# Optimization experiments

Hardware: AMD Instinct MI355X
Metric: run time of the kernel (lower is better)

Reference implementation:

```python
import jax, jax.numpy as jnp
import numpy as np

R = 1024          # number of 'a' tokens merged per sample
PROTECT_CLS = True


def setup_inputs() -> dict:
    key = jax.random.key(0)
    k1, k2 = jax.random.split(key)
    B, T, C = 8, 4096, 512
    x = jax.random.normal(k1, (B, T, C), dtype=jnp.float32)
    k = jax.random.normal(k2, (B, T, C), dtype=jnp.float32)
    return {"x": x, "k": k}


def reference(x, k):
    B, T, C = x.shape
    r = R
    pos_a = jnp.arange(0, T, 2)          # (Ta,)
    pos_b = jnp.arange(1, T, 2)          # (Tb,)
    Tb = pos_b.shape[0]

    # cosine-similarity scores between even ('a') and odd ('b') keys
    a = k[:, ::2, :]
    b = k[:, 1::2, :]
    a = a / (jnp.linalg.norm(a, axis=-1, keepdims=True) + 1e-12)
    b = b / (jnp.linalg.norm(b, axis=-1, keepdims=True) + 1e-12)
    scores = jnp.einsum('bac,bdc->bad', a, b)   # (B, Ta, Tb)
    if PROTECT_CLS:
        scores = scores.at[:, 0, :].set(-jnp.inf)

    node_max = jnp.max(scores, axis=-1)          # (B, Ta)
    node_idx = jnp.argmax(scores, axis=-1)       # (B, Ta) best 'b' partner per 'a'
    edge_order = jnp.argsort(-node_max, axis=-1) # descending
    src_idx = edge_order[:, :r]                  # merged 'a' tokens
    unm_sorted = jnp.sort(edge_order[:, r:], axis=-1)  # unmerged 'a', sorted
    dst_idx = jnp.take_along_axis(node_idx, src_idx, axis=-1)  # (B, r)

    src_tok = x[:, ::2, :]
    dst_tok = x[:, 1::2, :]
    unm = jnp.take_along_axis(src_tok, unm_sorted[..., None], axis=1)      # (B, Ta-r, C)
    src_sel = jnp.take_along_axis(src_tok, src_idx[..., None], axis=1)     # (B, r, C)
    dst_updated = jax.vmap(lambda d, i, s: d.at[i].add(s))(dst_tok, dst_idx, src_sel)
    merged = jnp.concatenate([unm, dst_updated], axis=1)                   # (B, Ta-r+Tb, C)

    base_b = unm.shape[1]
    unm_pos = pos_a[unm_sorted]   # (B, Ta-r) original positions of unmerged 'a'
    src_pos = pos_a[src_idx]      # (B, r)    original positions of merged 'a'

    def build_si(up, sp, di):
        si = jnp.full((T,), -1, dtype=jnp.int32)
        si = si.at[up].set(jnp.arange(base_b, dtype=jnp.int32))
        si = si.at[pos_b].set(base_b + jnp.arange(Tb, dtype=jnp.int32))
        si = si.at[sp].set((base_b + di).astype(jnp.int32))
        return si

    source_index = jax.vmap(build_si)(unm_pos, src_pos, dst_idx)  # (B, T)
    return merged, source_index
```

## Files before the change

kernel.cpp:

```cpp
#include <hip/hip_runtime.h>
#include <stdint.h>

#define BN 8
#define TN 4096
#define CN 512
#define TA 2048
#define RR 1024
#define BASEB 1024
#define MROWS 3072
#define KC 32

typedef _Float16 f16x8 __attribute__((ext_vector_type(8)));
typedef float f32x4 __attribute__((ext_vector_type(4)));
typedef __attribute__((address_space(3))) uint32_t lds_u32_t;
typedef __attribute__((address_space(1))) const uint32_t g_u32_t;

__device__ __forceinline__ unsigned ofloat(float f) {
    unsigned u = __float_as_uint(f);
    return (u & 0x80000000u) ? ~u : (u | 0x80000000u);
}

__global__ __launch_bounds__(256) void split_kernel(const float* __restrict__ k,
        _Float16* __restrict__ Ahi, _Float16* __restrict__ Alo,
        _Float16* __restrict__ Bhi, _Float16* __restrict__ Blo) {
    int row = blockIdx.x * 4 + (threadIdx.x >> 6);
    int lane = threadIdx.x & 63;
    const float* p = k + (size_t)row * CN;
    float4 v1 = *(const float4*)(p + lane * 8);
    float4 v2 = *(const float4*)(p + lane * 8 + 4);
    float s = v1.x*v1.x + v1.y*v1.y + v1.z*v1.z + v1.w*v1.w
            + v2.x*v2.x + v2.y*v2.y + v2.z*v2.z + v2.w*v2.w;
    #pragma unroll
    for (int off = 32; off > 0; off >>= 1) s += __shfl_xor(s, off);
    float sc = 1024.0f / (sqrtf(s) + 1e-12f);
    float m[8] = {v1.x*sc, v1.y*sc, v1.z*sc, v1.w*sc,
                  v2.x*sc, v2.y*sc, v2.z*sc, v2.w*sc};
    f16x8 H, L;
    #pragma unroll
    for (int jj = 0; jj < 8; ++jj) {
        _Float16 h = (_Float16)m[jj];
        H[jj] = h;
        L[jj] = (_Float16)(m[jj] - (float)h);
    }
    int b = row >> 12;
    int tt = row & 4095;
    size_t dst = ((size_t)(b * TA + (tt >> 1))) * CN + lane * 8;
    if (tt & 1) { *(f16x8*)(Bhi + dst) = H; *(f16x8*)(Blo + dst) = L; }
    else        { *(f16x8*)(Ahi + dst) = H; *(f16x8*)(Alo + dst) = L; }
}

__global__ void init_kernel(unsigned long long* __restrict__ nodekey) {
    int idx = blockIdx.x * 256 + threadIdx.x;
    if (idx < BN * TA)
        nodekey[idx] = (((unsigned long long)0x007FFFFFu) << 32) | 0xFFFFFFFFull;
}

__global__ __launch_bounds__(256, 4) void score_mfma_kernel(
        const _Float16* __restrict__ Ahi, const _Float16* __restrict__ Alo,
        const _Float16* __restrict__ Bhi, const _Float16* __restrict__ Blo,
        unsigned long long* __restrict__ nodekey) {
    __shared__ _Float16 lds[4 * 128 * KC];
    const int b  = blockIdx.z;
    const int i0 = blockIdx.x * 128;
    const int j0 = blockIdx.y * 128;
    const int tid = threadIdx.x;
    const int lane = tid & 63;
    const int w = tid >> 6;
    const int wr = (w >> 1) * 64;
    const int wc = (w & 1) * 64;
    const size_t boff = (size_t)b * TA * CN;

    const _Float16* gbase[4] = {
        Ahi + boff + (size_t)i0 * CN,
        Alo + boff + (size_t)i0 * CN,
        Bhi + boff + (size_t)j0 * CN,
        Blo + boff + (size_t)j0 * CN };

    const int srow = tid >> 2;
    const int segD = (tid & 3) ^ ((tid >> 3) & 3);

    f32x4 acc[4][4];
    #pragma unroll
    for (int m = 0; m < 4; ++m)
        #pragma unroll
        for (int n = 0; n < 4; ++n) acc[m][n] = (f32x4){0.f, 0.f, 0.f, 0.f};

    const int fr = lane & 15, ks = lane >> 4;
    int aoff[4], boff2[4];
    #pragma unroll
    for (int m = 0; m < 4; ++m) {
        int r = wr + m * 16 + fr;
        aoff[m] = r * KC + (ks ^ ((r >> 1) & 3)) * 8;
    }
    #pragma unroll
    for (int n = 0; n < 4; ++n) {
        int r = wc + n * 16 + fr;
        boff2[n] = r * KC + (ks ^ ((r >> 1) & 3)) * 8;
    }

    for (int kt = 0; kt < CN; kt += KC) {
        #pragma unroll
        for (int i = 0; i < 8; ++i) {
            const _Float16* gp = gbase[i >> 1]
                + (size_t)((i & 1) * 64 + srow) * CN + kt + segD * 8;
            _Float16* lp = lds + i * 2048 + w * 512;
            __builtin_amdgcn_global_load_lds((g_u32_t*)gp, (lds_u32_t*)lp, 16, 0, 0);
        }
        __syncthreads();
        f16x8 bh[4], bl[4];
        #pragma unroll
        for (int n = 0; n < 4; ++n) {
            bh[n] = *(const f16x8*)(&lds[2 * 4096 + boff2[n]]);
            bl[n] = *(const f16x8*)(&lds[3 * 4096 + boff2[n]]);
        }
        #pragma unroll
        for (int m = 0; m < 4; ++m) {
            f16x8 ah = *(const f16x8*)(&lds[0 * 4096 + aoff[m]]);
            f16x8 al = *(const f16x8*)(&lds[1 * 4096 + aoff[m]]);
            #pragma unroll
            for (int n = 0; n < 4; ++n) {
                acc[m][n] = __builtin_amdgcn_mfma_f32_16x16x32_f16(ah, bh[n], acc[m][n], 0, 0, 0);
                acc[m][n] = __builtin_amdgcn_mfma_f32_16x16x32_f16(ah, bl[n], acc[m][n], 0, 0, 0);
                acc[m][n] = __builtin_amdgcn_mfma_f32_16x16x32_f16(al, bh[n], acc[m][n], 0, 0, 0);
            }
        }
        __syncthreads();
    }

    const float SC = 1.0f / 1048576.0f;
    #pragma unroll
    for (int m = 0; m < 4; ++m) {
        #pragma unroll
        for (int reg = 0; reg < 4; ++reg) {
            unsigned bhi = 0u, blo2 = 0u;
            #pragma unroll
            for (int n = 0; n < 4; ++n) {
                float sc = acc[m][n][reg] * SC;
                unsigned j = (unsigned)(j0 + wc + n * 16 + fr);
                unsigned khi = ofloat(sc), klo = 0xFFFFFFFFu - j;
                if (khi > bhi || (khi == bhi && klo > blo2)) { bhi = khi; blo2 = klo; }
            }
            #pragma unroll
            for (int mm2 = 8; mm2 > 0; mm2 >>= 1) {
                unsigned ohi = (unsigned)__shfl_xor((int)bhi, mm2, 16);
                unsigned olo = (unsigned)__shfl_xor((int)blo2, mm2, 16);
                if (ohi > bhi || (ohi == bhi && olo > blo2)) { bhi = ohi; blo2 = olo; }
            }
            if (fr == 0) {
                int i = i0 + wr + m * 16 + ks * 4 + reg;
                if (i != 0) {
                    unsigned long long key = (((unsigned long long)bhi) << 32) | blo2;
                    atomicMax(&nodekey[b * TA + i], key);
                }
            }
        }
    }
}

__global__ __launch_bounds__(256) void rank_flag_kernel(
        const unsigned long long* __restrict__ nodekey,
        int* __restrict__ is_src) {
    __shared__ unsigned long long K[2048];
    const int b = blockIdx.y;
    const int t = threadIdx.x;
    for (int i = t; i < 2048; i += 256) {
        unsigned hi = (unsigned)(nodekey[b * TA + i] >> 32);
        K[i] = (((unsigned long long)hi) << 32) | (unsigned)(2047 - i);
    }
    __syncthreads();
    const int i = blockIdx.x * 256 + t;
    const unsigned long long ki = K[i];
    int rank = 0;
    #pragma unroll 8
    for (int j = 0; j < 2048; ++j) rank += (K[j] > ki) ? 1 : 0;
    is_src[b * TA + i] = (rank < RR) ? 1 : 0;
}

__global__ __launch_bounds__(1024) void scan_si_kernel(const int* __restrict__ is_src,
        const unsigned long long* __restrict__ nodekey,
        int* __restrict__ unm_rank, float* __restrict__ out_si) {
    __shared__ int ps[2048];
    __shared__ unsigned char fl[2048];
    const int b = blockIdx.x;
    const int t = threadIdx.x;
    int s0 = is_src[b * TA + t];
    int s1 = is_src[b * TA + 1024 + t];
    int f0 = 1 - s0, f1 = 1 - s1;
    fl[t] = (unsigned char)s0;
    fl[t + 1024] = (unsigned char)s1;
    ps[t] = f0;
    ps[t + 1024] = f1;
    __syncthreads();
    for (int off = 1; off < 2048; off <<= 1) {
        int v0 = (t >= off) ? ps[t - off] : 0;
        int v1 = ((t + 1024) >= off) ? ps[t + 1024 - off] : 0;
        __syncthreads();
        ps[t] += v0;
        ps[t + 1024] += v1;
        __syncthreads();
    }
    int u0 = ps[t] - f0, u1 = ps[t + 1024] - f1;
    unm_rank[b * TA + t] = u0;
    unm_rank[b * TA + 1024 + t] = u1;
    #pragma unroll
    for (int h = 0; h < 2; ++h) {
        int i = t + h * 1024;
        int u = h ? u1 : u0;
        int val;
        if (fl[i]) {
            unsigned j = 0xFFFFFFFFu - (unsigned)(nodekey[b * TA + i] & 0xFFFFFFFFull);
            val = BASEB + (int)j;
        } else {
            val = u;
        }
        out_si[(size_t)b * TN + 2 * i]     = (float)val;
        out_si[(size_t)b * TN + 2 * i + 1] = (float)(BASEB + i);
    }
}

__global__ __launch_bounds__(128) void copy_kernel(const float* __restrict__ x,
                                                   const int* __restrict__ is_src,
                                                   const int* __restrict__ unm_rank,
                                                   float* __restrict__ out) {
    const int b = blockIdx.y;
    const int tt = blockIdx.x;
    const float* src;
    float* dst;
    if (tt < 2048) {
        int i = tt;
        if (is_src[b * TA + i]) return;
        src = x + ((size_t)b * TN + 2 * i) * CN;
        dst = out + ((size_t)b * MROWS + unm_rank[b * TA + i]) * CN;
    } else {
        int j = tt - 2048;
        src = x + ((size_t)b * TN + 2 * j + 1) * CN;
        dst = out + ((size_t)b * MROWS + BASEB + j) * CN;
    }
    ((float4*)dst)[threadIdx.x] = ((const float4*)src)[threadIdx.x];
}

__global__ __launch_bounds__(256) void scatter_kernel(const float* __restrict__ x,
                                                      const int* __restrict__ is_src,
                                                      const unsigned long long* __restrict__ nodekey,
                                                      float* __restrict__ out) {
    const int b = blockIdx.y;
    const int i = blockIdx.x;
    if (!is_src[b * TA + i]) return;
    unsigned j = 0xFFFFFFFFu - (unsigned)(nodekey[b * TA + i] & 0xFFFFFFFFull);
    const float* src = x + ((size_t)b * TN + 2 * i) * CN;
    float* dst = out + ((size_t)b * MROWS + BASEB + j) * CN;
    for (int c = threadIdx.x; c < CN; c += 256) atomicAdd(&dst[c], src[c]);
}

extern "C" void kernel_launch(void* const* d_in, const int* in_sizes, int n_in,
                              void* d_out, int out_size, void* d_ws, size_t ws_size,
                              hipStream_t stream) {
    const float* x = (const float*)d_in[0];
    const float* k = (const float*)d_in[1];
    float* out = (float*)d_out;
    float* out_si = out + (size_t)BN * MROWS * CN;

    char* ws = (char*)d_ws;
    const size_t PLANE = (size_t)BN * TA * CN;
    _Float16* Ahi = (_Float16*)ws;
    _Float16* Alo = Ahi + PLANE;
    _Float16* Bhi = Alo + PLANE;
    _Float16* Blo = Bhi + PLANE;
    char* tail = ws + 4 * PLANE * sizeof(_Float16);
    unsigned long long* nodekey = (unsigned long long*)(tail);
    int* is_src   = (int*)(tail + 128 * 1024);
    int* unm_rank = (int*)(tail + 192 * 1024);

    split_kernel<<<dim3(BN * TN / 4), dim3(256), 0, stream>>>(k, Ahi, Alo, Bhi, Blo);
    init_kernel<<<dim3((BN * TA + 255) / 256), dim3(256), 0, stream>>>(nodekey);
    score_mfma_kernel<<<dim3(16, 16, BN), dim3(256), 0, stream>>>(Ahi, Alo, Bhi, Blo, nodekey);
    rank_flag_kernel<<<dim3(8, BN), dim3(256), 0, stream>>>(nodekey, is_src);
    scan_si_kernel<<<dim3(BN), dim3(1024), 0, stream>>>(is_src, nodekey, unm_rank, out_si);
    copy_kernel<<<dim3(4096, BN), dim3(128), 0, stream>>>(x, is_src, unm_rank, out);
    scatter_kernel<<<dim3(2048, BN), dim3(256), 0, stream>>>(x, is_src, nodekey, out);
}
```

Before: 204.8 us.

## Replace split-fp16 3-MFMA scoring with hi-only GEMM plus error-bounded candidate rescore

The score GEMM now uses only the high fp16 part of each normalized key (one MFMA instead of three per tile) and writes a tight row max. Using per-row error bounds built from the hi/lo norms, it keeps up to 64 candidate columns per row that could still be the true argmax. A new rescore kernel recomputes those candidates exactly in fp32 from the original keys, and falls back to a full scan when a row overflows. This cuts MFMA work and the lo-plane memory traffic, but adds candidate atomics, a second pass, and a risk of slow fallback rows.

```diff
diff --git a/kernel.cpp b/kernel.cpp
--- a/kernel.cpp
+++ b/kernel.cpp
@@ -9,6 +9,7 @@
 #define BASEB 1024
 #define MROWS 3072
 #define KC 32
+#define CAP 64
 
 typedef _Float16 f16x8 __attribute__((ext_vector_type(8)));
 typedef float f32x4 __attribute__((ext_vector_type(4)));
@@ -19,10 +20,16 @@
     unsigned u = __float_as_uint(f);
     return (u & 0x80000000u) ? ~u : (u | 0x80000000u);
 }
+__device__ __forceinline__ float unofloat(unsigned u) {
+    unsigned v = (u & 0x80000000u) ? (u ^ 0x80000000u) : ~u;
+    return __uint_as_float(v);
+}
 
 __global__ __launch_bounds__(256) void split_kernel(const float* __restrict__ k,
-        _Float16* __restrict__ Ahi, _Float16* __restrict__ Alo,
-        _Float16* __restrict__ Bhi, _Float16* __restrict__ Blo) {
+        _Float16* __restrict__ Ahi, _Float16* __restrict__ Bhi,
+        float* __restrict__ invA, float* __restrict__ invB,
+        float* __restrict__ nHa, float* __restrict__ nLa,
+        float* __restrict__ Pq, float* __restrict__ Qq) {
     int row = blockIdx.x * 4 + (threadIdx.x >> 6);
     int lane = threadIdx.x & 63;
     const float* p = k + (size_t)row * CN;
@@ -32,34 +39,66 @@
             + v2.x*v2.x + v2.y*v2.y + v2.z*v2.z + v2.w*v2.w;
     #pragma unroll
     for (int off = 32; off > 0; off >>= 1) s += __shfl_xor(s, off);
-    float sc = 1024.0f / (sqrtf(s) + 1e-12f);
+    float inv = 1.0f / (sqrtf(s) + 1e-12f);
+    float sc = 1024.0f * inv;
     float m[8] = {v1.x*sc, v1.y*sc, v1.z*sc, v1.w*sc,
                   v2.x*sc, v2.y*sc, v2.z*sc, v2.w*sc};
-    f16x8 H, L;
+    f16x8 H;
+    float h2 = 0.f, l2 = 0.f;
     #pragma unroll
     for (int jj = 0; jj < 8; ++jj) {
         _Float16 h = (_Float16)m[jj];
         H[jj] = h;
-        L[jj] = (_Float16)(m[jj] - (float)h);
-    }
+        float hf = (float)h;
+        float lf = m[jj] - hf;
+        h2 += hf * hf;
+        l2 += lf * lf;
+    }
+    #pragma unroll
+    for (int off = 32; off > 0; off >>= 1) {
+        h2 += __shfl_xor(h2, off);
+        l2 += __shfl_xor(l2, off);
+    }
+    float nh = sqrtf(h2), nl = sqrtf(l2);
     int b = row >> 12;
     int tt = row & 4095;
-    size_t dst = ((size_t)(b * TA + (tt >> 1))) * CN + lane * 8;
-    if (tt & 1) { *(f16x8*)(Bhi + dst) = H; *(f16x8*)(Blo + dst) = L; }
-    else        { *(f16x8*)(Ahi + dst) = H; *(f16x8*)(Alo + dst) = L; }
-}
-
-__global__ void init_kernel(unsigned long long* __restrict__ nodekey) {
+    int node = tt >> 1;
+    size_t dst = ((size_t)(b * TA + node)) * CN + lane * 8;
+    if (tt & 1) {
+        *(f16x8*)(Bhi + dst) = H;
+        if (lane == 0) {
+            invB[b * TA + node] = inv;
+            Pq[b * TA + node] = nl + 1.2f + 4e-5f * nh;
+            Qq[b * TA + node] = nh + nl + 1050.0f;
+        }
+    } else {
+        *(f16x8*)(Ahi + dst) = H;
+        if (lane == 0) {
+            invA[b * TA + node] = inv;
+            nHa[b * TA + node] = nh;
+            nLa[b * TA + node] = nl;
+        }
+    }
+}
+
+__global__ void init_kernel(unsigned long long* __restrict__ nodekey,
+                            int* __restrict__ cnt, unsigned* __restrict__ maxHH) {
     int idx = blockIdx.x * 256 + threadIdx.x;
-    if (idx < BN * TA)
+    if (idx < BN * TA) {
         nodekey[idx] = (((unsigned long long)0x007FFFFFu) << 32) | 0xFFFFFFFFull;
-}
-
-__global__ __launch_bounds__(256, 4) void score_mfma_kernel(
-        const _Float16* __restrict__ Ahi, const _Float16* __restrict__ Alo,
-        const _Float16* __restrict__ Bhi, const _Float16* __restrict__ Blo,
-        unsigned long long* __restrict__ nodekey) {
-    __shared__ _Float16 lds[4 * 128 * KC];
+        cnt[idx] = 0;
+        maxHH[idx] = 0u;
+    }
+}
+
+__global__ __launch_bounds__(256, 4) void score_hh_kernel(
+        const _Float16* __restrict__ Ahi, const _Float16* __restrict__ Bhi,
+        const float* __restrict__ nHa, const float* __restrict__ nLa,
+        const float* __restrict__ Pq, const float* __restrict__ Qq,
+        int* __restrict__ cnt, unsigned* __restrict__ maxHH,
+        int* __restrict__ candJ, float* __restrict__ candS) {
+    __shared__ _Float16 lds[2 * 128 * KC];
+    __shared__ float rowmax2[128][2];
     const int b  = blockIdx.z;
     const int i0 = blockIdx.x * 128;
     const int j0 = blockIdx.y * 128;
@@ -70,11 +109,8 @@
     const int wc = (w & 1) * 64;
     const size_t boff = (size_t)b * TA * CN;
 
-    const _Float16* gbase[4] = {
-        Ahi + boff + (size_t)i0 * CN,
-        Alo + boff + (size_t)i0 * CN,
-        Bhi + boff + (size_t)j0 * CN,
-        Blo + boff + (size_t)j0 * CN };
+    const _Float16* gbase[2] = { Ahi + boff + (size_t)i0 * CN,
+                                 Bhi + boff + (size_t)j0 * CN };
 
     const int srow = tid >> 2;
     const int segD = (tid & 3) ^ ((tid >> 3) & 3);
@@ -100,61 +136,142 @@
 
     for (int kt = 0; kt < CN; kt += KC) {
         #pragma unroll
-        for (int i = 0; i < 8; ++i) {
+        for (int i = 0; i < 4; ++i) {
             const _Float16* gp = gbase[i >> 1]
                 + (size_t)((i & 1) * 64 + srow) * CN + kt + segD * 8;
             _Float16* lp = lds + i * 2048 + w * 512;
             __builtin_amdgcn_global_load_lds((g_u32_t*)gp, (lds_u32_t*)lp, 16, 0, 0);
         }
         __syncthreads();
-        f16x8 bh[4], bl[4];
-        #pragma unroll
-        for (int n = 0; n < 4; ++n) {
-            bh[n] = *(const f16x8*)(&lds[2 * 4096 + boff2[n]]);
-            bl[n] = *(const f16x8*)(&lds[3 * 4096 + boff2[n]]);
-        }
+        f16x8 bh[4];
+        #pragma unroll
+        for (int n = 0; n < 4; ++n)
+            bh[n] = *(const f16x8*)(&lds[4096 + boff2[n]]);
         #pragma unroll
         for (int m = 0; m < 4; ++m) {
-            f16x8 ah = *(const f16x8*)(&lds[0 * 4096 + aoff[m]]);
-            f16x8 al = *(const f16x8*)(&lds[1 * 4096 + aoff[m]]);
+            f16x8 ah = *(const f16x8*)(&lds[aoff[m]]);
+            #pragma unroll
+            for (int n = 0; n < 4; ++n)
+                acc[m][n] = __builtin_amdgcn_mfma_f32_16x16x32_f16(ah, bh[n], acc[m][n], 0, 0, 0);
+        }
+        __syncthreads();
+    }
+
+    float wmax[4][4];
+    #pragma unroll
+    for (int m = 0; m < 4; ++m)
+        #pragma unroll
+        for (int reg = 0; reg < 4; ++reg) {
+            float mx = acc[m][0][reg];
+            #pragma unroll
+            for (int n = 1; n < 4; ++n) mx = fmaxf(mx, acc[m][n][reg]);
+            #pragma unroll
+            for (int mm2 = 8; mm2 > 0; mm2 >>= 1)
+                mx = fmaxf(mx, __shfl_xor(mx, mm2, 16));
+            wmax[m][reg] = mx;
+        }
+    if (fr == 0) {
+        #pragma unroll
+        for (int m = 0; m < 4; ++m)
+            #pragma unroll
+            for (int reg = 0; reg < 4; ++reg) {
+                int r = wr + m * 16 + ks * 4 + reg;
+                rowmax2[r][w & 1] = wmax[m][reg];
+            }
+    }
+    __syncthreads();
+    if (fr == 0) {
+        #pragma unroll
+        for (int m = 0; m < 4; ++m)
+            #pragma unroll
+            for (int reg = 0; reg < 4; ++reg) {
+                int r = wr + m * 16 + ks * 4 + reg;
+                atomicMax(&maxHH[b * TA + i0 + r], ofloat(wmax[m][reg]));
+            }
+    }
+    float Pj[4], Qj[4];
+    #pragma unroll
+    for (int n = 0; n < 4; ++n) {
+        int j = j0 + wc + n * 16 + fr;
+        Pj[n] = Pq[b * TA + j];
+        Qj[n] = Qq[b * TA + j];
+    }
+    #pragma unroll
+    for (int m = 0; m < 4; ++m)
+        #pragma unroll
+        for (int reg = 0; reg < 4; ++reg) {
+            int r = wr + m * 16 + ks * 4 + reg;
+            int i = i0 + r;
+            float M = fmaxf(rowmax2[r][0], rowmax2[r][1]);
+            float ha = nHa[b * TA + i], la = nLa[b * TA + i];
             #pragma unroll
             for (int n = 0; n < 4; ++n) {
-                acc[m][n] = __builtin_amdgcn_mfma_f32_16x16x32_f16(ah, bh[n], acc[m][n], 0, 0, 0);
-                acc[m][n] = __builtin_amdgcn_mfma_f32_16x16x32_f16(ah, bl[n], acc[m][n], 0, 0, 0);
-                acc[m][n] = __builtin_amdgcn_mfma_f32_16x16x32_f16(al, bh[n], acc[m][n], 0, 0, 0);
-            }
-        }
-        __syncthreads();
-    }
-
-    const float SC = 1.0f / 1048576.0f;
-    #pragma unroll
-    for (int m = 0; m < 4; ++m) {
-        #pragma unroll
-        for (int reg = 0; reg < 4; ++reg) {
-            unsigned bhi = 0u, blo2 = 0u;
-            #pragma unroll
-            for (int n = 0; n < 4; ++n) {
-                float sc = acc[m][n][reg] * SC;
-                unsigned j = (unsigned)(j0 + wc + n * 16 + fr);
-                unsigned khi = ofloat(sc), klo = 0xFFFFFFFFu - j;
-                if (khi > bhi || (khi == bhi && klo > blo2)) { bhi = khi; blo2 = klo; }
-            }
-            #pragma unroll
-            for (int mm2 = 8; mm2 > 0; mm2 >>= 1) {
-                unsigned ohi = (unsigned)__shfl_xor((int)bhi, mm2, 16);
-                unsigned olo = (unsigned)__shfl_xor((int)blo2, mm2, 16);
-                if (ohi > bhi || (ohi == bhi && olo > blo2)) { bhi = ohi; blo2 = olo; }
-            }
-            if (fr == 0) {
-                int i = i0 + wr + m * 16 + ks * 4 + reg;
-                if (i != 0) {
-                    unsigned long long key = (((unsigned long long)bhi) << 32) | blo2;
-                    atomicMax(&nodekey[b * TA + i], key);
+                float s = acc[m][n][reg];
+                if (s >= M - (ha * Pj[n] + la * Qj[n])) {
+                    int j = j0 + wc + n * 16 + fr;
+                    int idx = atomicAdd(&cnt[b * TA + i], 1);
+                    if (idx < CAP) {
+                        candJ[(size_t)(b * TA + i) * CAP + idx] = j;
+                        candS[(size_t)(b * TA + i) * CAP + idx] = s;
+                    }
                 }
             }
         }
-    }
+}
+
+__global__ __launch_bounds__(256) void rescore_kernel(const float* __restrict__ k,
+        const float* __restrict__ invA, const float* __restrict__ invB,
+        const float* __restrict__ nHa, const float* __restrict__ nLa,
+        const float* __restrict__ Pq, const float* __restrict__ Qq,
+        const int* __restrict__ cnt, const unsigned* __restrict__ maxHH,
+        const int* __restrict__ candJ, const float* __restrict__ candS,
+        unsigned long long* __restrict__ nodekey) {
+    const int b = blockIdx.y;
+    const int wv = threadIdx.x >> 6;
+    const int lane = threadIdx.x & 63;
+    const int i = blockIdx.x * 4 + wv;
+    if (i == 0) return;
+    const size_t base = (size_t)b * TA;
+    float inva = invA[base + i];
+    const float* ka = k + ((size_t)b * TN + 2 * i) * CN + lane * 8;
+    float a[8];
+    #pragma unroll
+    for (int e = 0; e < 8; ++e) a[e] = ka[e] * inva;
+    int c_n = cnt[base + i];
+    float gmax = unofloat(maxHH[base + i]);
+    float ha = nHa[base + i], la = nLa[base + i];
+    unsigned bhi = 0u, blo = 0u;
+
+    if (c_n <= CAP) {
+        for (int c = 0; c < c_n; ++c) {
+            int j = candJ[(base + i) * CAP + c];
+            float s = candS[(base + i) * CAP + c];
+            if (s < gmax - (ha * Pq[base + j] + la * Qq[base + j])) continue;
+            float invb = invB[base + j];
+            const float* kb = k + ((size_t)b * TN + 2 * j + 1) * CN + lane * 8;
+            float d = 0.f;
+            #pragma unroll
+            for (int e = 0; e < 8; ++e) d += a[e] * (kb[e] * invb);
+            #pragma unroll
+            for (int off = 32; off > 0; off >>= 1) d += __shfl_xor(d, off);
+            unsigned khi = ofloat(d), klo = 0xFFFFFFFFu - (unsigned)j;
+            if (khi > bhi || (khi == bhi && klo > blo)) { bhi = khi; blo = klo; }
+        }
+    } else {
+        for (int j = 0; j < TA; ++j) {
+            float invb = invB[base + j];
+            const float* kb = k + ((size_t)b * TN + 2 * j + 1) * CN + lane * 8;
+            float d = 0.f;
+            #pragma unroll
+            for (int e = 0; e < 8; ++e) d += a[e] * (kb[e] * invb);
+            #pragma unroll
+            for (int off = 32; off > 0; off >>= 1) d += __shfl_xor(d, off);
+            unsigned khi = ofloat(d), klo = 0xFFFFFFFFu - (unsigned)j;
+            if (khi > bhi || (khi == bhi && klo > blo)) { bhi = khi; blo = klo; }
+        }
+    }
+    if (lane == 0)
+        nodekey[base + i] = (((unsigned long long)bhi) << 32) | blo;
 }
 
 __global__ __launch_bounds__(256) void rank_flag_kernel(
@@ -263,17 +380,30 @@
     char* ws = (char*)d_ws;
     const size_t PLANE = (size_t)BN * TA * CN;
     _Float16* Ahi = (_Float16*)ws;
-    _Float16* Alo = Ahi + PLANE;
-    _Float16* Bhi = Alo + PLANE;
-    _Float16* Blo = Bhi + PLANE;
-    char* tail = ws + 4 * PLANE * sizeof(_Float16);
-    unsigned long long* nodekey = (unsigned long long*)(tail);
-    int* is_src   = (int*)(tail + 128 * 1024);
-    int* unm_rank = (int*)(tail + 192 * 1024);
-
-    split_kernel<<<dim3(BN * TN / 4), dim3(256), 0, stream>>>(k, Ahi, Alo, Bhi, Blo);
-    init_kernel<<<dim3((BN * TA + 255) / 256), dim3(256), 0, stream>>>(nodekey);
-    score_mfma_kernel<<<dim3(16, 16, BN), dim3(256), 0, stream>>>(Ahi, Alo, Bhi, Blo, nodekey);
+    _Float16* Bhi = Ahi + PLANE;
+    char* tail = ws + 2 * PLANE * sizeof(_Float16);
+    const size_t NN = (size_t)BN * TA;
+    float* invA = (float*)(tail);
+    float* invB = invA + NN;
+    float* nHa  = invB + NN;
+    float* nLa  = nHa + NN;
+    float* Pq   = nLa + NN;
+    float* Qq   = Pq + NN;
+    unsigned long long* nodekey = (unsigned long long*)(Qq + NN);
+    int* cnt        = (int*)(nodekey + NN);
+    unsigned* maxHH = (unsigned*)(cnt + NN);
+    int* is_src     = (int*)(maxHH + NN);
+    int* unm_rank   = is_src + NN;
+    int* candJ      = unm_rank + NN;
+    float* candS    = (float*)(candJ + NN * CAP);
+
+    split_kernel<<<dim3(BN * TN / 4), dim3(256), 0, stream>>>(
+        k, Ahi, Bhi, invA, invB, nHa, nLa, Pq, Qq);
+    init_kernel<<<dim3((BN * TA + 255) / 256), dim3(256), 0, stream>>>(nodekey, cnt, maxHH);
+    score_hh_kernel<<<dim3(16, 16, BN), dim3(256), 0, stream>>>(
+        Ahi, Bhi, nHa, nLa, Pq, Qq, cnt, maxHH, candJ, candS);
+    rescore_kernel<<<dim3(512, BN), dim3(256), 0, stream>>>(
+        k, invA, invB, nHa, nLa, Pq, Qq, cnt, maxHH, candJ, candS, nodekey);
     rank_flag_kernel<<<dim3(8, BN), dim3(256), 0, stream>>>(nodekey, is_src);
     scan_si_kernel<<<dim3(BN), dim3(1024), 0, stream>>>(is_src, nodekey, unm_rank, out_si);
     copy_kernel<<<dim3(4096, BN), dim3(128), 0, stream>>>(x, is_src, unm_rank, out);
```

Result: slower. 209.6 us (+2.3%).
